# Performance work log

Measured on AMD Instinct MI355X. Metric: run time of the kernel, lower is better.

## Reference

```python
import jax, jax.numpy as jnp
import numpy as np

EPS = 1e-5
D_CONV = 4


def rmsnorm(x, w):
    return x * jax.lax.rsqrt(jnp.mean(x * x, axis=-1, keepdims=True) + EPS) * w


def layernorm(x, w, b):
    m = jnp.mean(x, axis=-1, keepdims=True)
    v = jnp.mean((x - m) ** 2, axis=-1, keepdims=True)
    return (x - m) * jax.lax.rsqrt(v + EPS) * w + b


def mamba_mixer(x, W_in, conv_w, conv_b, W_x, W_dt, b_dt, A_log, Dp, W_out):
    # x: [B, L, C]; HF MambaMixer slow path (selective scan)
    B, L, C = x.shape
    I = W_out.shape[1]          # intermediate_size = expand*C
    N = A_log.shape[1]          # state_size
    R = W_dt.shape[1]           # time_step_rank
    proj = x @ W_in.T                                   # [B,L,2I]
    hs, gate = jnp.split(proj, 2, axis=-1)
    # causal depthwise conv over L (kernel D_CONV, left pad D_CONV-1)
    hs_c = jax.lax.conv_general_dilated(
        hs.transpose(0, 2, 1), conv_w, (1,), [(D_CONV - 1, 0)],
        dimension_numbers=("NCH", "OIH", "NCH"), feature_group_count=I)
    hs = jax.nn.silu(hs_c.transpose(0, 2, 1) + conv_b)  # [B,L,I]
    ssm_in = hs @ W_x.T                                 # [B,L,R+2N]
    dt_r, Bm, Cm = jnp.split(ssm_in, [R, R + N], axis=-1)
    dt = jax.nn.softplus(dt_r @ W_dt.T + b_dt)          # [B,L,I]
    A = -jnp.exp(A_log)                                 # [I,N]

    def step(state, inp):
        dt_t, B_t, C_t, u_t = inp                       # [B,I],[B,N],[B,N],[B,I]
        dA = jnp.exp(dt_t[:, :, None] * A)              # [B,I,N]
        state = dA * state + dt_t[:, :, None] * B_t[:, None, :] * u_t[:, :, None]
        y = jnp.einsum("bin,bn->bi", state, C_t)
        return state, y

    xs = (dt.transpose(1, 0, 2), Bm.transpose(1, 0, 2),
          Cm.transpose(1, 0, 2), hs.transpose(1, 0, 2))
    state0 = jnp.zeros((B, I, N), x.dtype)
    _, ys = jax.lax.scan(step, state0, xs)              # ys: [L,B,I]
    y = ys.transpose(1, 0, 2) + hs * Dp                 # skip term D*u
    y = y * jax.nn.silu(gate)
    return y @ W_out.T                                  # [B,L,C]


def forward_scan(x, W_in, conv_w, conv_b, W_x, W_dt, b_dt, A_log, Dp, W_out,
                 rms_w1, rms_wf):
    # HF MambaModel, 1 layer: residual + mixer(rmsnorm(x)), then final rmsnorm
    h = x + mamba_mixer(rmsnorm(x, rms_w1), W_in, conv_w, conv_b, W_x, W_dt,
                        b_dt, A_log, Dp, W_out)
    return rmsnorm(h, rms_wf)


def setup_inputs() -> dict:
    key = jax.random.key(0)
    ks = jax.random.split(key, 12)
    BT, H, W, C = 8, 32, 32, 256
    I, N, R = 2 * C, 16, 16  # intermediate, state, time_step_rank=ceil(C/16)
    s = 0.02
    x = jax.random.normal(ks[0], (BT, H, W, C), jnp.float32)
    W_in = jax.random.normal(ks[1], (2 * I, C), jnp.float32) * s
    conv_w = jax.random.normal(ks[2], (I, 1, D_CONV), jnp.float32) * s
    conv_b = jax.random.normal(ks[3], (I,), jnp.float32) * s
    W_x = jax.random.normal(ks[4], (R + 2 * N, I), jnp.float32) * s
    W_dt = jax.random.normal(ks[5], (I, R), jnp.float32) * s
    b_dt = jax.random.normal(ks[6], (I,), jnp.float32) * 0.1
    A_log = jnp.log(jnp.broadcast_to(jnp.arange(1, N + 1, dtype=jnp.float32), (I, N)))
    Dp = jnp.ones((I,), jnp.float32)
    W_out = jax.random.normal(ks[7], (C, I), jnp.float32) * s
    rms_w1 = jnp.ones((C,), jnp.float32)
    rms_wf = jnp.ones((C,), jnp.float32)
    ln_w = jnp.ones((C,), jnp.float32)
    ln_b = jnp.zeros((C,), jnp.float32)
    return {"x": x, "W_in": W_in, "conv_w": conv_w, "conv_b": conv_b,
            "W_x": W_x, "W_dt": W_dt, "b_dt": b_dt, "A_log": A_log, "Dp": Dp,
            "W_out": W_out, "rms_w1": rms_w1, "rms_wf": rms_wf,
            "ln_w": ln_w, "ln_b": ln_b}


def reference(x, W_in, conv_w, conv_b, W_x, W_dt, b_dt, A_log, Dp, W_out,
              rms_w1, rms_wf, ln_w, ln_b):
    BT, H, W, C = x.shape
    # 4 scan directions stacked into the batch dim
    xs = jnp.stack([x, x[:, :, ::-1], x[:, ::-1], x[:, ::-1, ::-1]], axis=0)
    xs = xs.reshape(4 * BT, H * W, C)
    out = forward_scan(xs, W_in, conv_w, conv_b, W_x, W_dt, b_dt, A_log, Dp,
                       W_out, rms_w1, rms_wf)
    out = out.reshape(4, BT, H, W, C)
    o = (out[0] + out[1][:, :, ::-1] + out[2][:, ::-1]
         + out[3][:, ::-1, ::-1]) / 4.0
    return layernorm(o, ln_w, ln_b)
```

## Files before the change

### kernel.cpp

```cpp
#include <hip/hip_runtime.h>
#include <hip/hip_bf16.h>
#include <hip/hip_fp16.h>

#define EPSF 1e-5f
typedef __attribute__((ext_vector_type(8))) short short8;
typedef __attribute__((ext_vector_type(4))) float f32x4;
typedef __attribute__((ext_vector_type(2))) float f32x2;

__device__ __forceinline__ int map_tok(int d, int bt, int t) {
    int h = t >> 5, w = t & 31;
    if (d & 2) h = 31 - h;
    if (d & 1) w = 31 - w;
    return (bt << 10) + (h << 5) + w;
}

__device__ __forceinline__ float bf2f(unsigned short u) {
    unsigned int x = (unsigned int)u << 16;
    return __builtin_bit_cast(float, x);
}

__device__ __forceinline__ float wave_sum(float v) {
    #pragma unroll
    for (int m = 32; m >= 1; m >>= 1) v += __shfl_xor(v, m);
    return v;
}

__device__ __forceinline__ void softplus_pair(float z, float& dtv, float& e1) {
    float t = __expf(-fabsf(z));
    float r = __builtin_amdgcn_rcpf(1.f + t);
    e1 = (z >= 0.f) ? t * r : r;
    dtv = fmaxf(z, 0.f) + __logf(1.f + t);
}

__global__ __launch_bounds__(256)
void cvt_bf16_kernel(const float* __restrict__ in, __hip_bfloat16* __restrict__ out, int n) {
    int i = blockIdx.x * 256 + threadIdx.x;
    if (i < n) out[i] = __float2bfloat16(in[i]);
}

__global__ __launch_bounds__(256)
void cvt_pad_kernel(const float* __restrict__ in, __hip_bfloat16* __restrict__ out,
                    int n_real, int n_total) {
    int i = blockIdx.x * 256 + threadIdx.x;
    if (i < n_total) out[i] = __float2bfloat16(i < n_real ? in[i] : 0.f);
}

__global__ __launch_bounds__(256)
void rmsnorm_kernel(const float* __restrict__ x, const float* __restrict__ w,
                    __hip_bfloat16* __restrict__ xn) {
    int wave = threadIdx.x >> 6, lane = threadIdx.x & 63;
    int tok = blockIdx.x * 4 + wave;
    int c = lane * 4;
    float4 xv = *(const float4*)&x[(size_t)tok * 256 + c];
    float ss = wave_sum(xv.x * xv.x + xv.y * xv.y + xv.z * xv.z + xv.w * xv.w);
    float r = rsqrtf(ss * (1.f / 256.f) + EPSF);
    float4 wv = *(const float4*)&w[c];
    __hip_bfloat16 o[4];
    o[0] = __float2bfloat16(xv.x * r * wv.x);
    o[1] = __float2bfloat16(xv.y * r * wv.y);
    o[2] = __float2bfloat16(xv.z * r * wv.z);
    o[3] = __float2bfloat16(xv.w * r * wv.w);
    *(ushort4*)&xn[(size_t)tok * 256 + c] = *(ushort4*)o;
}

template <int BN, typename TO>
__global__ __launch_bounds__(256)
void gemm_mfma_lds(const __hip_bfloat16* __restrict__ A, int lda,
                   const __hip_bfloat16* __restrict__ B, int ldb,
                   TO* __restrict__ C, int ldc, int K) {
    constexpr int FN = BN / 64;
    constexpr int SLOTS = (64 + BN) * 4;
    constexpr int ITER = SLOTS / 256;
    __shared__ __hip_bfloat16 lds[(size_t)(64 + BN) * 32];
    int tid = threadIdx.x;
    int wave = tid >> 6, lane = tid & 63;
    int fr = lane & 15, kg = lane >> 4;
    int bm = blockIdx.x * 64;
    int bn = blockIdx.y * BN;
    f32x4 acc[4][FN] = {};
    for (int k0 = 0; k0 < K; k0 += 32) {
        __syncthreads();
        #pragma unroll
        for (int j = 0; j < ITER; ++j) {
            int slot = j * 256 + tid;
            short8 v;
            if (j == 0) {
                int row = slot >> 2, ko = slot & 3;
                v = *(const short8*)(A + (size_t)(bm + row) * lda + k0 + ko * 8);
            } else {
                int s2 = slot - 256;
                int row = s2 >> 2, ko = s2 & 3;
                v = *(const short8*)(B + (size_t)(bn + row) * ldb + k0 + ko * 8);
            }
            *(short8*)&lds[(size_t)slot * 8] = v;
        }
        __syncthreads();
        short8 af[4], bfr[FN];
        #pragma unroll
        for (int m = 0; m < 4; ++m)
            af[m] = *(const short8*)&lds[(size_t)((m * 16 + fr) * 32 + kg * 8)];
        #pragma unroll
        for (int n = 0; n < FN; ++n)
            bfr[n] = *(const short8*)&lds[(size_t)(2048 + (wave * (BN / 4) + n * 16 + fr) * 32 + kg * 8)];
        #pragma unroll
        for (int m = 0; m < 4; ++m)
            #pragma unroll
            for (int n = 0; n < FN; ++n)
                acc[m][n] = __builtin_amdgcn_mfma_f32_16x16x32_bf16(af[m], bfr[n], acc[m][n], 0, 0, 0);
    }
    #pragma unroll
    for (int m = 0; m < 4; ++m) {
        int crow = bm + m * 16 + kg * 4;
        #pragma unroll
        for (int n = 0; n < FN; ++n) {
            int ccol = bn + wave * (BN / 4) + n * 16 + fr;
            #pragma unroll
            for (int r = 0; r < 4; ++r) {
                if constexpr (sizeof(TO) == 4)
                    C[(size_t)(crow + r) * ldc + ccol] = acc[m][n][r];
                else
                    C[(size_t)(crow + r) * ldc + ccol] = __float2bfloat16(acc[m][n][r]);
            }
        }
    }
}

__global__ __launch_bounds__(256)
void conv_silu_kernel(const __hip_bfloat16* __restrict__ proj,
                      const float* __restrict__ conv_w,
                      const float* __restrict__ conv_b,
                      __hip_bfloat16* __restrict__ hs_cb) {
    int tb = blockIdx.x;
    int s = blockIdx.y;
    int tid = threadIdx.x;
    int i0 = tid * 2;
    int d = s >> 3, bt = s & 7;
    int t0 = tb * 16;
    float4 w0 = *(const float4*)&conv_w[i0 * 4];
    float4 w1 = *(const float4*)&conv_w[i0 * 4 + 4];
    float b0 = conv_b[i0], b1 = conv_b[i0 + 1];
    float pa0 = 0.f, pa1 = 0.f, pb0 = 0.f, pb1 = 0.f, pc0 = 0.f, pc1 = 0.f;
    #pragma unroll
    for (int k = 0; k < 3; ++k) {
        int tt = t0 - 3 + k;
        if (tt >= 0) {
            int tok = map_tok(d, bt, tt);
            ushort2 v = *(const ushort2*)(proj + (size_t)tok * 1024 + i0);
            if (k == 0) { pa0 = bf2f(v.x); pa1 = bf2f(v.y); }
            else if (k == 1) { pb0 = bf2f(v.x); pb1 = bf2f(v.y); }
            else { pc0 = bf2f(v.x); pc1 = bf2f(v.y); }
        }
    }
    for (int t = t0; t < t0 + 16; ++t) {
        int tok = map_tok(d, bt, t);
        ushort2 v = *(const ushort2*)(proj + (size_t)tok * 1024 + i0);
        float pd0 = bf2f(v.x), pd1 = bf2f(v.y);
        float acc0 = b0;
        acc0 = fmaf(w0.x, pa0, acc0); acc0 = fmaf(w0.y, pb0, acc0);
        acc0 = fmaf(w0.z, pc0, acc0); acc0 = fmaf(w0.w, pd0, acc0);
        float acc1 = b1;
        acc1 = fmaf(w1.x, pa1, acc1); acc1 = fmaf(w1.y, pb1, acc1);
        acc1 = fmaf(w1.z, pc1, acc1); acc1 = fmaf(w1.w, pd1, acc1);
        float v0 = acc0 * __builtin_amdgcn_rcpf(1.f + __expf(-acc0));
        float v1 = acc1 * __builtin_amdgcn_rcpf(1.f + __expf(-acc1));
        __hip_bfloat16 o[2] = {__float2bfloat16(v0), __float2bfloat16(v1)};
        *(ushort2*)(hs_cb + ((size_t)s * 1024 + t) * 512 + i0) = *(ushort2*)o;
        pa0 = pb0; pb0 = pc0; pc0 = pd0;
        pa1 = pb1; pb1 = pc1; pc1 = pd1;
    }
}

__global__ __launch_bounds__(256)
void scan_pass1(const __hip_bfloat16* __restrict__ hs_cb,
                const float* __restrict__ ssm,
                const float* __restrict__ W_dt,
                const float* __restrict__ b_dt,
                const float* __restrict__ Dp,
                __hip_bfloat16* __restrict__ y_locb,
                __half* __restrict__ qh,
                __hip_bfloat16* __restrict__ localfinal,
                __hip_bfloat16* __restrict__ decayprod) {
    __shared__ float sZ[32][64];
    int tid = threadIdx.x;
    int blk = blockIdx.x;
    int chunk = blk & 31;
    int s = blk >> 5;
    int i0 = tid * 2;
    int row0 = s * 1024 + chunk * 32;
    {
        int t = tid >> 4, c4 = tid & 15;
        *(float4*)&sZ[t][c4 * 4] = *(const float4*)&ssm[(size_t)(row0 + t) * 64 + c4 * 4];
        t = (tid + 256) >> 4; c4 = (tid + 256) & 15;
        *(float4*)&sZ[t][c4 * 4] = *(const float4*)&ssm[(size_t)(row0 + t) * 64 + c4 * 4];
    }
    __syncthreads();
    f32x2 wdt[16];
    #pragma unroll
    for (int q = 0; q < 4; ++q) {
        float4 wa = *(const float4*)&W_dt[i0 * 16 + q * 4];
        float4 wb = *(const float4*)&W_dt[(i0 + 1) * 16 + q * 4];
        wdt[q * 4 + 0] = (f32x2){wa.x, wb.x};
        wdt[q * 4 + 1] = (f32x2){wa.y, wb.y};
        wdt[q * 4 + 2] = (f32x2){wa.z, wb.z};
        wdt[q * 4 + 3] = (f32x2){wa.w, wb.w};
    }
    float2 bd = *(const float2*)&b_dt[i0];
    float2 dv2 = *(const float2*)&Dp[i0];
    f32x2 bdt = {bd.x, bd.y};
    f32x2 Dv = {dv2.x, dv2.y};
    f32x2 st[16];
    #pragma unroll
    for (int n = 0; n < 16; ++n) st[n] = (f32x2){0.f, 0.f};
    const __hip_bfloat16* us = hs_cb + (size_t)row0 * 512;
    __hip_bfloat16* yl = y_locb + (size_t)row0 * 512;
    __half* qs = qh + (size_t)row0 * 512;
    f32x2 qd = {1.f, 1.f};
    for (int t = 0; t < 32; ++t) {
        f32x2 z = bdt;
        #pragma unroll
        for (int n = 0; n < 16; ++n) z += wdt[n] * sZ[t][n];
        float dtvA, e1A, dtvB, e1B;
        softplus_pair(z.x, dtvA, e1A);
        softplus_pair(z.y, dtvB, e1B);
        f32x2 e1 = {e1A, e1B};
        ushort2 uv = *(const ushort2*)(us + t * 512 + i0);
        f32x2 u = {bf2f(uv.x), bf2f(uv.y)};
        f32x2 dtu = (f32x2){dtvA, dtvB} * u;
        qd *= e1;
        f32x2 dA = e1;
        f32x2 y = {0.f, 0.f};
        #pragma unroll
        for (int q = 0; q < 4; ++q) {
            float4 b4 = *(const float4*)&sZ[t][16 + q * 4];
            float4 c4 = *(const float4*)&sZ[t][32 + q * 4];
            float br[4] = {b4.x, b4.y, b4.z, b4.w};
            float cr[4] = {c4.x, c4.y, c4.z, c4.w};
            #pragma unroll
            for (int m = 0; m < 4; ++m) {
                int n = q * 4 + m;
                st[n] = dA * st[n] + dtu * br[m];
                y += st[n] * cr[m];
                dA *= e1;
            }
        }
        y += u * Dv;
        __hip_bfloat16 yo[2] = {__float2bfloat16(y.x), __float2bfloat16(y.y)};
        *(ushort2*)(yl + t * 512 + i0) = *(ushort2*)yo;
        __half qo[2] = {__float2half(qd.x), __float2half(qd.y)};
        *(ushort2*)(qs + t * 512 + i0) = *(ushort2*)qo;
    }
    f32x2 p = qd;
    size_t base = (((size_t)s * 32 + chunk) * 16) * 512 + i0;
    #pragma unroll
    for (int n = 0; n < 16; ++n) {
        __hip_bfloat16 lo[2] = {__float2bfloat16(st[n].x), __float2bfloat16(st[n].y)};
        *(ushort2*)(localfinal + base + (size_t)n * 512) = *(ushort2*)lo;
        __hip_bfloat16 po[2] = {__float2bfloat16(p.x), __float2bfloat16(p.y)};
        *(ushort2*)(decayprod + base + (size_t)n * 512) = *(ushort2*)po;
        p *= qd;
    }
}

__global__ __launch_bounds__(256)
void scan_pass2(__hip_bfloat16* __restrict__ localfinal,
                const __hip_bfloat16* __restrict__ decayprod) {
    int g = blockIdx.x * 256 + threadIdx.x;
    int s = g >> 13;
    int r = g & 8191;
    float carry = 0.f;
    for (int c = 0; c < 32; ++c) {
        size_t idx = ((size_t)s * 32 + c) * 8192 + r;
        float lf = __bfloat162float(localfinal[idx]);
        float p  = __bfloat162float(decayprod[idx]);
        localfinal[idx] = __float2bfloat16(carry);
        carry = fmaf(p, carry, lf);
    }
}

__global__ __launch_bounds__(256)
void scan_pass3(const __hip_bfloat16* __restrict__ y_locb,
                const __half* __restrict__ qh,
                const float* __restrict__ ssm,
                const __hip_bfloat16* __restrict__ proj,
                const __hip_bfloat16* __restrict__ initstate,
                __hip_bfloat16* __restrict__ y_actb) {
    __shared__ float sC[32][16];
    int tid = threadIdx.x;
    int blk = blockIdx.x;
    int chunk = blk & 31;
    int s = blk >> 5;
    int i0 = tid * 2;
    int d = s >> 3, bt = s & 7;
    int row0 = s * 1024 + chunk * 32;
    if (tid < 128) {
        int t = tid >> 2, c4 = tid & 3;
        *(float4*)&sC[t][c4 * 4] = *(const float4*)&ssm[(size_t)(row0 + t) * 64 + 32 + c4 * 4];
    }
    __syncthreads();
    f32x2 si[16];
    size_t ibase = (((size_t)s * 32 + chunk) * 16) * 512 + i0;
    #pragma unroll
    for (int n = 0; n < 16; ++n) {
        ushort2 sv = *(const ushort2*)(initstate + ibase + (size_t)n * 512);
        si[n] = (f32x2){bf2f(sv.x), bf2f(sv.y)};
    }
    const __hip_bfloat16* yl = y_locb + (size_t)row0 * 512;
    const __half* qs = qh + (size_t)row0 * 512;
    __hip_bfloat16* ys = y_actb + (size_t)row0 * 512;
    int t0 = chunk * 32;
    for (int t = 0; t < 32; ++t) {
        ushort2 yv2 = *(const ushort2*)(yl + t * 512 + i0);
        f32x2 yv = {bf2f(yv2.x), bf2f(yv2.y)};
        __half2 hq = *(const __half2*)(qs + t * 512 + i0);
        f32x2 qv = {__half2float(hq.x), __half2float(hq.y)};
        f32x2 acc = si[15] * sC[t][15];
        #pragma unroll
        for (int n = 14; n >= 0; --n) acc = acc * qv + si[n] * sC[t][n];
        f32x2 corr = acc * qv;
        int tok = map_tok(d, bt, t0 + t);
        ushort2 gv = *(const ushort2*)(proj + (size_t)tok * 1024 + 512 + i0);
        float gx = bf2f(gv.x), gy = bf2f(gv.y);
        f32x2 sg = {gx * __builtin_amdgcn_rcpf(1.f + __expf(-gx)),
                    gy * __builtin_amdgcn_rcpf(1.f + __expf(-gy))};
        f32x2 ov = (yv + corr) * sg;
        __hip_bfloat16 oo[2] = {__float2bfloat16(ov.x), __float2bfloat16(ov.y)};
        *(ushort2*)(ys + t * 512 + i0) = *(ushort2*)oo;
    }
}

__global__ __launch_bounds__(256)
void combine_kernel(const float* __restrict__ x,
                    const __hip_bfloat16* __restrict__ mixb,
                    const float* __restrict__ rms_wf,
                    const float* __restrict__ ln_w,
                    const float* __restrict__ ln_b,
                    float* __restrict__ out) {
    int wave = threadIdx.x >> 6, lane = threadIdx.x & 63;
    int tok = blockIdx.x * 4 + wave;
    int c = lane * 4;
    int bt = tok >> 10;
    int hw = tok & 1023;
    int h = hw >> 5, w = hw & 31;
    float4 xv = *(const float4*)&x[(size_t)tok * 256 + c];
    float4 wf = *(const float4*)&rms_wf[c];
    float o[4] = {0.f, 0.f, 0.f, 0.f};
    #pragma unroll
    for (int d = 0; d < 4; ++d) {
        int hh = (d & 2) ? 31 - h : h;
        int ww = (d & 1) ? 31 - w : w;
        int t = (hh << 5) + ww;
        ushort4 mu = *(const ushort4*)&mixb[(((size_t)d * 8 + bt) * 1024 + t) * 256 + c];
        float hv[4] = {xv.x + bf2f(mu.x), xv.y + bf2f(mu.y),
                       xv.z + bf2f(mu.z), xv.w + bf2f(mu.w)};
        float ss = wave_sum(hv[0] * hv[0] + hv[1] * hv[1] + hv[2] * hv[2] + hv[3] * hv[3]);
        float r = rsqrtf(ss * (1.f / 256.f) + EPSF);
        float wfr[4] = {wf.x, wf.y, wf.z, wf.w};
        #pragma unroll
        for (int j = 0; j < 4; ++j) o[j] = fmaf(hv[j] * r, wfr[j], o[j]);
    }
    #pragma unroll
    for (int j = 0; j < 4; ++j) o[j] *= 0.25f;
    float m = wave_sum(o[0] + o[1] + o[2] + o[3]) * (1.f / 256.f);
    float dv[4] = {o[0] - m, o[1] - m, o[2] - m, o[3] - m};
    float var = wave_sum(dv[0] * dv[0] + dv[1] * dv[1] + dv[2] * dv[2] + dv[3] * dv[3]) * (1.f / 256.f);
    float rs = rsqrtf(var + EPSF);
    float4 lw = *(const float4*)&ln_w[c];
    float4 lb = *(const float4*)&ln_b[c];
    float4 ov;
    ov.x = fmaf(dv[0] * rs, lw.x, lb.x);
    ov.y = fmaf(dv[1] * rs, lw.y, lb.y);
    ov.z = fmaf(dv[2] * rs, lw.z, lb.z);
    ov.w = fmaf(dv[3] * rs, lw.w, lb.w);
    *(float4*)&out[(size_t)tok * 256 + c] = ov;
}

extern "C" void kernel_launch(void* const* d_in, const int* in_sizes, int n_in,
                              void* d_out, int out_size, void* d_ws, size_t ws_size,
                              hipStream_t stream) {
    const float* x      = (const float*)d_in[0];
    const float* W_in   = (const float*)d_in[1];
    const float* conv_w = (const float*)d_in[2];
    const float* conv_b = (const float*)d_in[3];
    const float* W_x    = (const float*)d_in[4];
    const float* W_dt   = (const float*)d_in[5];
    const float* b_dt   = (const float*)d_in[6];
    const float* Dp     = (const float*)d_in[8];
    const float* W_out  = (const float*)d_in[9];
    const float* rms_w1 = (const float*)d_in[10];
    const float* rms_wf = (const float*)d_in[11];
    const float* ln_w   = (const float*)d_in[12];
    const float* ln_b   = (const float*)d_in[13];

    float* ws = (float*)d_ws;
    __hip_bfloat16* mixb   = (__hip_bfloat16*)ws;
    __hip_bfloat16* projb  = (__hip_bfloat16*)(ws + 8388608);
    __hip_bfloat16* hs_cb  = (__hip_bfloat16*)(ws + 12582912);
    __hip_bfloat16* y_actb = (__hip_bfloat16*)(ws + 20971520);
    float* ssm             = ws + 29360128;
    __hip_bfloat16* lf     = (__hip_bfloat16*)(ws + 31457280);
    __hip_bfloat16* dp     = (__hip_bfloat16*)(ws + 35651584);
    __hip_bfloat16* W_inb  = (__hip_bfloat16*)(ws + 39845888);
    __hip_bfloat16* W_xb   = (__hip_bfloat16*)(ws + 39976960);
    __hip_bfloat16* W_outb = (__hip_bfloat16*)(ws + 39993344);
    __hip_bfloat16* y_locb = (__hip_bfloat16*)(ws + 40058880);
    __half* qh             = (__half*)(ws + 48447488);
    __hip_bfloat16* xn = y_actb;

    cvt_bf16_kernel<<<1024, 256, 0, stream>>>(W_in, W_inb, 262144);
    cvt_pad_kernel<<<128, 256, 0, stream>>>(W_x, W_xb, 24576, 32768);
    cvt_bf16_kernel<<<512, 256, 0, stream>>>(W_out, W_outb, 131072);

    rmsnorm_kernel<<<2048, 256, 0, stream>>>(x, rms_w1, xn);
    gemm_mfma_lds<256, __hip_bfloat16><<<dim3(128, 4), 256, 0, stream>>>(
        xn, 256, W_inb, 256, projb, 1024, 256);
    conv_silu_kernel<<<dim3(64, 32), 256, 0, stream>>>(projb, conv_w, conv_b, hs_cb);
    gemm_mfma_lds<64, float><<<dim3(512, 1), 256, 0, stream>>>(
        hs_cb, 512, W_xb, 512, ssm, 64, 512);
    scan_pass1<<<1024, 256, 0, stream>>>(hs_cb, ssm, W_dt, b_dt, Dp, y_locb, qh, lf, dp);
    scan_pass2<<<1024, 256, 0, stream>>>(lf, dp);
    scan_pass3<<<1024, 256, 0, stream>>>(y_locb, qh, ssm, projb, lf, y_actb);
    gemm_mfma_lds<256, __hip_bfloat16><<<dim3(512, 1), 256, 0, stream>>>(
        y_actb, 512, W_outb, 512, mixb, 256, 512);
    combine_kernel<<<2048, 256, 0, stream>>>(x, mixb, rms_wf, ln_w, ln_b, (float*)d_out);
}
```

Baseline: 155.7 us.

## Fold W_dt into W_x and compute dt via MFMA GEMM with fused softplus

Precomputes W_eff = W_dt·W_x[:R] so the dt projection becomes a direct 512x512 bf16 MFMA GEMM from hs, with softplus and exp-decay fused into its epilogue and stored as bf16/fp16 arrays. The scan's first pass then loads dt and e1 instead of doing a rank-16 dot product and transcendentals per step, and the x-projection GEMM now only produces B and C. It also splits the y accumulation into four partial sums to shorten the dependency chain, and reshuffles the workspace layout. In exchange it adds a larger GEMM plus extra memory traffic for the dt and e1 tensors, and lowers the precision of the values fed to the scan.

```diff
diff --git a/kernel.cpp b/kernel.cpp
--- a/kernel.cpp
+++ b/kernel.cpp
@@ -25,13 +25,6 @@
     return v;
 }
 
-__device__ __forceinline__ void softplus_pair(float z, float& dtv, float& e1) {
-    float t = __expf(-fabsf(z));
-    float r = __builtin_amdgcn_rcpf(1.f + t);
-    e1 = (z >= 0.f) ? t * r : r;
-    dtv = fmaxf(z, 0.f) + __logf(1.f + t);
-}
-
 __global__ __launch_bounds__(256)
 void cvt_bf16_kernel(const float* __restrict__ in, __hip_bfloat16* __restrict__ out, int n) {
     int i = blockIdx.x * 256 + threadIdx.x;
@@ -43,6 +36,18 @@
                     int n_real, int n_total) {
     int i = blockIdx.x * 256 + threadIdx.x;
     if (i < n_total) out[i] = __float2bfloat16(i < n_real ? in[i] : 0.f);
+}
+
+__global__ __launch_bounds__(256)
+void weff_kernel(const float* __restrict__ W_dt, const float* __restrict__ W_x,
+                 __hip_bfloat16* __restrict__ W_effb) {
+    int gid = blockIdx.x * 256 + threadIdx.x;
+    int i = gid >> 9, j = gid & 511;
+    float acc = 0.f;
+    #pragma unroll
+    for (int r = 0; r < 16; ++r)
+        acc = fmaf(W_dt[i * 16 + r], W_x[r * 512 + j], acc);
+    W_effb[gid] = __float2bfloat16(acc);
 }
 
 __global__ __launch_bounds__(256)
@@ -120,6 +125,72 @@
                     C[(size_t)(crow + r) * ldc + ccol] = acc[m][n][r];
                 else
                     C[(size_t)(crow + r) * ldc + ccol] = __float2bfloat16(acc[m][n][r]);
+            }
+        }
+    }
+}
+
+__global__ __launch_bounds__(256)
+void gemm_dt(const __hip_bfloat16* __restrict__ A,
+             const __hip_bfloat16* __restrict__ B,
+             const float* __restrict__ b_dt,
+             __hip_bfloat16* __restrict__ dtb,
+             __half* __restrict__ e1h) {
+    constexpr int BN = 256, FN = 4, ITER = 5;
+    __shared__ __hip_bfloat16 lds[(size_t)(64 + BN) * 32];
+    int tid = threadIdx.x;
+    int wave = tid >> 6, lane = tid & 63;
+    int fr = lane & 15, kg = lane >> 4;
+    int bm = blockIdx.x * 64;
+    int bn = blockIdx.y * BN;
+    f32x4 acc[4][FN] = {};
+    for (int k0 = 0; k0 < 512; k0 += 32) {
+        __syncthreads();
+        #pragma unroll
+        for (int j = 0; j < ITER; ++j) {
+            int slot = j * 256 + tid;
+            short8 v;
+            if (j == 0) {
+                int row = slot >> 2, ko = slot & 3;
+                v = *(const short8*)(A + (size_t)(bm + row) * 512 + k0 + ko * 8);
+            } else {
+                int s2 = slot - 256;
+                int row = s2 >> 2, ko = s2 & 3;
+                v = *(const short8*)(B + (size_t)(bn + row) * 512 + k0 + ko * 8);
+            }
+            *(short8*)&lds[(size_t)slot * 8] = v;
+        }
+        __syncthreads();
+        short8 af[4], bfr[FN];
+        #pragma unroll
+        for (int m = 0; m < 4; ++m)
+            af[m] = *(const short8*)&lds[(size_t)((m * 16 + fr) * 32 + kg * 8)];
+        #pragma unroll
+        for (int n = 0; n < FN; ++n)
+            bfr[n] = *(const short8*)&lds[(size_t)(2048 + (wave * 64 + n * 16 + fr) * 32 + kg * 8)];
+        #pragma unroll
+        for (int m = 0; m < 4; ++m)
+            #pragma unroll
+            for (int n = 0; n < FN; ++n)
+                acc[m][n] = __builtin_amdgcn_mfma_f32_16x16x32_bf16(af[m], bfr[n], acc[m][n], 0, 0, 0);
+    }
+    #pragma unroll
+    for (int m = 0; m < 4; ++m) {
+        int crow = bm + m * 16 + kg * 4;
+        #pragma unroll
+        for (int n = 0; n < FN; ++n) {
+            int ccol = bn + wave * 64 + n * 16 + fr;
+            float bdt = b_dt[ccol];
+            #pragma unroll
+            for (int r = 0; r < 4; ++r) {
+                float z = acc[m][n][r] + bdt;
+                float t_ = __expf(-fabsf(z));
+                float rc = __builtin_amdgcn_rcpf(1.f + t_);
+                float e1 = (z >= 0.f) ? t_ * rc : rc;
+                float dtv = fmaxf(z, 0.f) + __logf(1.f + t_);
+                size_t off = (size_t)(crow + r) * 512 + ccol;
+                dtb[off] = __float2bfloat16(dtv);
+                e1h[off] = __float2half(e1);
             }
         }
     }
@@ -172,15 +243,15 @@
 
 __global__ __launch_bounds__(256)
 void scan_pass1(const __hip_bfloat16* __restrict__ hs_cb,
+                const __hip_bfloat16* __restrict__ dtb,
+                const __half* __restrict__ e1h,
                 const float* __restrict__ ssm,
-                const float* __restrict__ W_dt,
-                const float* __restrict__ b_dt,
                 const float* __restrict__ Dp,
                 __hip_bfloat16* __restrict__ y_locb,
                 __half* __restrict__ qh,
                 __hip_bfloat16* __restrict__ localfinal,
                 __hip_bfloat16* __restrict__ decayprod) {
-    __shared__ float sZ[32][64];
+    __shared__ float sZ[32][32];
     int tid = threadIdx.x;
     int blk = blockIdx.x;
     int chunk = blk & 31;
@@ -188,62 +259,48 @@
     int i0 = tid * 2;
     int row0 = s * 1024 + chunk * 32;
     {
-        int t = tid >> 4, c4 = tid & 15;
-        *(float4*)&sZ[t][c4 * 4] = *(const float4*)&ssm[(size_t)(row0 + t) * 64 + c4 * 4];
-        t = (tid + 256) >> 4; c4 = (tid + 256) & 15;
-        *(float4*)&sZ[t][c4 * 4] = *(const float4*)&ssm[(size_t)(row0 + t) * 64 + c4 * 4];
+        int t = tid >> 3, q = tid & 7;
+        *(float4*)&sZ[t][q * 4] = *(const float4*)&ssm[(size_t)(row0 + t) * 64 + q * 4];
     }
     __syncthreads();
-    f32x2 wdt[16];
-    #pragma unroll
-    for (int q = 0; q < 4; ++q) {
-        float4 wa = *(const float4*)&W_dt[i0 * 16 + q * 4];
-        float4 wb = *(const float4*)&W_dt[(i0 + 1) * 16 + q * 4];
-        wdt[q * 4 + 0] = (f32x2){wa.x, wb.x};
-        wdt[q * 4 + 1] = (f32x2){wa.y, wb.y};
-        wdt[q * 4 + 2] = (f32x2){wa.z, wb.z};
-        wdt[q * 4 + 3] = (f32x2){wa.w, wb.w};
-    }
-    float2 bd = *(const float2*)&b_dt[i0];
     float2 dv2 = *(const float2*)&Dp[i0];
-    f32x2 bdt = {bd.x, bd.y};
     f32x2 Dv = {dv2.x, dv2.y};
     f32x2 st[16];
     #pragma unroll
     for (int n = 0; n < 16; ++n) st[n] = (f32x2){0.f, 0.f};
     const __hip_bfloat16* us = hs_cb + (size_t)row0 * 512;
+    const __hip_bfloat16* dts = dtb + (size_t)row0 * 512;
+    const __half* es = e1h + (size_t)row0 * 512;
     __hip_bfloat16* yl = y_locb + (size_t)row0 * 512;
     __half* qs = qh + (size_t)row0 * 512;
     f32x2 qd = {1.f, 1.f};
     for (int t = 0; t < 32; ++t) {
-        f32x2 z = bdt;
-        #pragma unroll
-        for (int n = 0; n < 16; ++n) z += wdt[n] * sZ[t][n];
-        float dtvA, e1A, dtvB, e1B;
-        softplus_pair(z.x, dtvA, e1A);
-        softplus_pair(z.y, dtvB, e1B);
-        f32x2 e1 = {e1A, e1B};
+        ushort2 dv = *(const ushort2*)(dts + t * 512 + i0);
+        f32x2 dtv = {bf2f(dv.x), bf2f(dv.y)};
+        __half2 ev = *(const __half2*)(es + t * 512 + i0);
+        f32x2 e1 = {__half2float(ev.x), __half2float(ev.y)};
         ushort2 uv = *(const ushort2*)(us + t * 512 + i0);
         f32x2 u = {bf2f(uv.x), bf2f(uv.y)};
-        f32x2 dtu = (f32x2){dtvA, dtvB} * u;
+        f32x2 dtu = dtv * u;
         qd *= e1;
         f32x2 dA = e1;
-        f32x2 y = {0.f, 0.f};
+        f32x2 yq[4] = {(f32x2){0.f, 0.f}, (f32x2){0.f, 0.f},
+                       (f32x2){0.f, 0.f}, (f32x2){0.f, 0.f}};
         #pragma unroll
         for (int q = 0; q < 4; ++q) {
-            float4 b4 = *(const float4*)&sZ[t][16 + q * 4];
-            float4 c4 = *(const float4*)&sZ[t][32 + q * 4];
+            float4 b4 = *(const float4*)&sZ[t][q * 4];
+            float4 c4 = *(const float4*)&sZ[t][16 + q * 4];
             float br[4] = {b4.x, b4.y, b4.z, b4.w};
             float cr[4] = {c4.x, c4.y, c4.z, c4.w};
             #pragma unroll
             for (int m = 0; m < 4; ++m) {
                 int n = q * 4 + m;
                 st[n] = dA * st[n] + dtu * br[m];
-                y += st[n] * cr[m];
+                yq[q] += st[n] * cr[m];
                 dA *= e1;
             }
         }
-        y += u * Dv;
+        f32x2 y = (yq[0] + yq[1]) + (yq[2] + yq[3]) + u * Dv;
         __hip_bfloat16 yo[2] = {__float2bfloat16(y.x), __float2bfloat16(y.y)};
         *(ushort2*)(yl + t * 512 + i0) = *(ushort2*)yo;
         __half qo[2] = {__float2half(qd.x), __float2half(qd.y)};
@@ -294,7 +351,7 @@
     int row0 = s * 1024 + chunk * 32;
     if (tid < 128) {
         int t = tid >> 2, c4 = tid & 3;
-        *(float4*)&sC[t][c4 * 4] = *(const float4*)&ssm[(size_t)(row0 + t) * 64 + 32 + c4 * 4];
+        *(float4*)&sC[t][c4 * 4] = *(const float4*)&ssm[(size_t)(row0 + t) * 64 + 16 + c4 * 4];
     }
     __syncthreads();
     f32x2 si[16];
@@ -392,31 +449,36 @@
     const float* ln_b   = (const float*)d_in[13];
 
     float* ws = (float*)d_ws;
-    __hip_bfloat16* mixb   = (__hip_bfloat16*)ws;
-    __hip_bfloat16* projb  = (__hip_bfloat16*)(ws + 8388608);
-    __hip_bfloat16* hs_cb  = (__hip_bfloat16*)(ws + 12582912);
-    __hip_bfloat16* y_actb = (__hip_bfloat16*)(ws + 20971520);
-    float* ssm             = ws + 29360128;
+    __hip_bfloat16* projb  = (__hip_bfloat16*)ws;
+    __hip_bfloat16* hs_cb  = (__hip_bfloat16*)(ws + 4194304);
+    float* ssm             = ws + 12582912;
+    __hip_bfloat16* dtb    = (__hip_bfloat16*)(ws + 14680064);
+    __half* e1h            = (__half*)(ws + 23068672);
     __hip_bfloat16* lf     = (__hip_bfloat16*)(ws + 31457280);
     __hip_bfloat16* dp     = (__hip_bfloat16*)(ws + 35651584);
-    __hip_bfloat16* W_inb  = (__hip_bfloat16*)(ws + 39845888);
-    __hip_bfloat16* W_xb   = (__hip_bfloat16*)(ws + 39976960);
-    __hip_bfloat16* W_outb = (__hip_bfloat16*)(ws + 39993344);
-    __hip_bfloat16* y_locb = (__hip_bfloat16*)(ws + 40058880);
-    __half* qh             = (__half*)(ws + 48447488);
-    __hip_bfloat16* xn = y_actb;
+    __hip_bfloat16* y_locb = (__hip_bfloat16*)(ws + 39845888);
+    __half* qh             = (__half*)(ws + 48234496);
+    __hip_bfloat16* W_inb  = (__hip_bfloat16*)(ws + 56623104);
+    __hip_bfloat16* W_xb2  = (__hip_bfloat16*)(ws + 56754176);
+    __hip_bfloat16* W_outb = (__hip_bfloat16*)(ws + 56770560);
+    __hip_bfloat16* W_effb = (__hip_bfloat16*)(ws + 56836096);
+    __hip_bfloat16* xn     = y_locb;
+    __hip_bfloat16* y_actb = hs_cb;
+    __hip_bfloat16* mixb   = dp;
 
     cvt_bf16_kernel<<<1024, 256, 0, stream>>>(W_in, W_inb, 262144);
-    cvt_pad_kernel<<<128, 256, 0, stream>>>(W_x, W_xb, 24576, 32768);
+    cvt_pad_kernel<<<128, 256, 0, stream>>>(W_x + 8192, W_xb2, 16384, 32768);
     cvt_bf16_kernel<<<512, 256, 0, stream>>>(W_out, W_outb, 131072);
+    weff_kernel<<<1024, 256, 0, stream>>>(W_dt, W_x, W_effb);
 
     rmsnorm_kernel<<<2048, 256, 0, stream>>>(x, rms_w1, xn);
     gemm_mfma_lds<256, __hip_bfloat16><<<dim3(128, 4), 256, 0, stream>>>(
         xn, 256, W_inb, 256, projb, 1024, 256);
     conv_silu_kernel<<<dim3(64, 32), 256, 0, stream>>>(projb, conv_w, conv_b, hs_cb);
     gemm_mfma_lds<64, float><<<dim3(512, 1), 256, 0, stream>>>(
-        hs_cb, 512, W_xb, 512, ssm, 64, 512);
-    scan_pass1<<<1024, 256, 0, stream>>>(hs_cb, ssm, W_dt, b_dt, Dp, y_locb, qh, lf, dp);
+        hs_cb, 512, W_xb2, 512, ssm, 64, 512);
+    gemm_dt<<<dim3(512, 2), 256, 0, stream>>>(hs_cb, W_effb, b_dt, dtb, e1h);
+    scan_pass1<<<1024, 256, 0, stream>>>(hs_cb, dtb, e1h, ssm, Dp, y_locb, qh, lf, dp);
     scan_pass2<<<1024, 256, 0, stream>>>(lf, dp);
     scan_pass3<<<1024, 256, 0, stream>>>(y_locb, qh, ssm, projb, lf, y_actb);
     gemm_mfma_lds<256, __hip_bfloat16><<<dim3(512, 1), 256, 0, stream>>>(
```

Measured after the change: 191.2 us. 1.23x slower.
